# Kernel optimization log

Hardware: AMD Instinct MI355X
Metric: run time of the kernel (lower is better)

The kernel has to match this reference:

```python
import jax, jax.numpy as jnp
import numpy as np

N = 50000        # nodes
E = 800000       # edges (avg degree 16)
F_IN = 128       # in_channels
HID = 32         # hidden_channels per head
H = 8            # heads
DH = HID * H     # 256, concat dim
NC = {'TL': 12, 'YL': 30, 'TS': 60, 'TZ': 120}
NEG_SLOPE = 0.2  # PyG GATConv default


def setup_inputs() -> dict:
    key = jax.random.key(0)
    ks = jax.random.split(key, 40)
    rn = lambda k, s, sc=0.1: jax.random.normal(k, s, jnp.float32) * sc
    inp = {}
    inp['x'] = jax.random.normal(ks[0], (N, F_IN), jnp.float32)
    inp['edge_index'] = jax.random.randint(ks[1], (2, E), 0, N, dtype=jnp.int64)
    # conv1: in -> H x HID (concat)
    inp['W1'] = rn(ks[2], (F_IN, DH)); inp['a1s'] = rn(ks[3], (H, HID)); inp['a1d'] = rn(ks[4], (H, HID)); inp['b1'] = jnp.zeros((DH,), jnp.float32)
    # conv2: DH -> H x HID (concat)
    inp['W2'] = rn(ks[5], (DH, DH)); inp['a2s'] = rn(ks[6], (H, HID)); inp['a2d'] = rn(ks[7], (H, HID)); inp['b2'] = jnp.zeros((DH,), jnp.float32)
    # task heads: DH -> C, heads=1, concat=False
    i = 8
    for t, c in NC.items():
        inp['W_' + t] = rn(ks[i], (DH, c)); i += 1
        inp['as_' + t] = rn(ks[i], (1, c)); i += 1
        inp['ad_' + t] = rn(ks[i], (1, c)); i += 1
        inp['b_' + t] = jnp.zeros((c,), jnp.float32)
    return inp


def gat_conv(x, src, dst, W, a_s, a_d, b, concat):
    """PyG-style GATConv (eval mode, self-loops already in src/dst)."""
    n = x.shape[0]
    heads, out_ch = a_s.shape
    h = (x @ W).reshape(n, heads, out_ch)                 # [N,H,C]
    alpha_s = jnp.einsum('nhc,hc->nh', h, a_s)            # [N,H]
    alpha_d = jnp.einsum('nhc,hc->nh', h, a_d)
    e = jax.nn.leaky_relu(alpha_s[src] + alpha_d[dst], NEG_SLOPE)   # [E,H]
    # numerically-stable segment softmax over incoming edges of each dst
    m = jax.ops.segment_max(e, dst, num_segments=n)
    ex = jnp.exp(e - m[dst])
    denom = jax.ops.segment_sum(ex, dst, num_segments=n)
    alpha = ex / (denom[dst] + 1e-16)                     # [E,H]
    out = jax.ops.segment_sum(alpha[:, :, None] * h[src], dst, num_segments=n)  # [N,H,C]
    out = out.reshape(n, heads * out_ch) if concat else out.mean(axis=1)
    return out + b


def reference(x, edge_index, W1, a1s, a1d, b1, W2, a2s, a2d, b2,
              W_TL, as_TL, ad_TL, b_TL, W_YL, as_YL, ad_YL, b_YL,
              W_TS, as_TS, ad_TS, b_TS, W_TZ, as_TZ, ad_TZ, b_TZ):
    n = x.shape[0]
    loop = jnp.arange(n, dtype=edge_index.dtype)
    src = jnp.concatenate([edge_index[0], loop])
    dst = jnp.concatenate([edge_index[1], loop])
    h = jax.nn.elu(gat_conv(x, src, dst, W1, a1s, a1d, b1, True))
    h = gat_conv(h, src, dst, W2, a2s, a2d, b2, True)
    tl = jax.nn.log_softmax(gat_conv(h, src, dst, W_TL, as_TL, ad_TL, b_TL, False), axis=1)
    yl = jax.nn.log_softmax(gat_conv(h, src, dst, W_YL, as_YL, ad_YL, b_YL, False), axis=1)
    ts = jax.nn.log_softmax(gat_conv(h, src, dst, W_TS, as_TS, ad_TS, b_TS, False), axis=1)
    tz = jax.nn.log_softmax(gat_conv(h, src, dst, W_TZ, as_TZ, ad_TZ, b_TZ, False), axis=1)
    return (tl, yl, ts, tz)
```

## Files before the change

kernel.cpp:

```cpp
#include <hip/hip_runtime.h>
#include <math.h>


#define NEG_SLOPE 0.2f

typedef short s8v __attribute__((ext_vector_type(8)));
typedef short s4v __attribute__((ext_vector_type(4)));
typedef float f4v __attribute__((ext_vector_type(4)));

__device__ __forceinline__ short f2bf(float x) {
    unsigned u = __float_as_uint(x);
    u += 0x7fffu + ((u >> 16) & 1u);
    return (short)(u >> 16);
}
__device__ __forceinline__ float bf2f(short b) {
    return __uint_as_float(((unsigned)(unsigned short)b) << 16);
}
__device__ __forceinline__ void split2(float x, short& h, short& l) {
    h = f2bf(x);
    l = f2bf(x - bf2f(h));
}
__device__ __forceinline__ float4 bf4_to_f4(s4v v) {
    return make_float4(bf2f(v[0]), bf2f(v[1]), bf2f(v[2]), bf2f(v[3]));
}


__global__ void init_kernel(int* __restrict__ deg, int* __restrict__ cursor, int n) {
    int i = blockIdx.x * blockDim.x + threadIdx.x;
    if (i < n) { deg[i] = 1; cursor[i] = 0; }
}

__global__ void count_kernel(const int* __restrict__ dst, int* __restrict__ deg, int E) {
    int i = blockIdx.x * blockDim.x + threadIdx.x;
    if (i < E) atomicAdd(&deg[dst[i]], 1);
}

__global__ __launch_bounds__(1024) void scan_kernel(const int* __restrict__ deg,
                                                    int* __restrict__ rowstart, int n) {
    __shared__ int sh[1024];
    __shared__ int carry_sh;
    if (threadIdx.x == 0) { carry_sh = 0; rowstart[0] = 0; }
    __syncthreads();
    for (int base = 0; base < n; base += 8192) {
        int vals[8];
        int sum = 0;
        int i0 = base + threadIdx.x * 8;
        #pragma unroll
        for (int j = 0; j < 8; ++j) {
            int i = i0 + j;
            int v = (i < n) ? deg[i] : 0;
            sum += v;
            vals[j] = sum;
        }
        sh[threadIdx.x] = sum;
        __syncthreads();
        for (int off = 1; off < 1024; off <<= 1) {
            int t = (threadIdx.x >= (unsigned)off) ? sh[threadIdx.x - off] : 0;
            __syncthreads();
            sh[threadIdx.x] += t;
            __syncthreads();
        }
        int excl = sh[threadIdx.x] - sum + carry_sh;
        #pragma unroll
        for (int j = 0; j < 8; ++j) {
            int i = i0 + j;
            if (i < n) rowstart[i + 1] = excl + vals[j];
        }
        __syncthreads();
        if (threadIdx.x == 0) carry_sh += sh[1023];
        __syncthreads();
    }
}

__global__ void scatter_kernel(const int* __restrict__ src, const int* __restrict__ dst,
                               const int* __restrict__ rowstart, int* __restrict__ cursor,
                               int* __restrict__ csr, int* __restrict__ csrd, int E, int n) {
    int i = blockIdx.x * blockDim.x + threadIdx.x;
    if (i >= E + n) return;
    int s, d;
    if (i < E) { s = src[i]; d = dst[i]; }
    else       { s = d = i - E; }
    int p = atomicAdd(&cursor[d], 1);
    int slot = rowstart[d] + p;
    csr[slot] = s;
    csrd[slot] = d;
}


__global__ void tobf_kernel(const float* __restrict__ A, short* __restrict__ Ah, int n4) {
    int i = blockIdx.x * blockDim.x + threadIdx.x;
    if (i >= n4) return;
    float4 v = ((const float4*)A)[i];
    s4v hv = {f2bf(v.x), f2bf(v.y), f2bf(v.z), f2bf(v.w)};
    ((s4v*)Ah)[i] = hv;
}

__global__ void split_bt_kernel(const float* __restrict__ B, short* __restrict__ Bh,
                                short* __restrict__ Bl, int K, int Nc, int kshift) {
    int idx = blockIdx.x * blockDim.x + threadIdx.x;
    if (idx >= Nc * K) return;
    int n = idx >> kshift;
    int k = idx & (K - 1);
    float v = B[(size_t)k * Nc + n];
    short h, l; split2(v, h, l);
    Bh[idx] = h;
    Bl[idx] = l;
}

__global__ void fold_alpha8_kernel(const float* __restrict__ W,
                                   const float* __restrict__ a_s, const float* __restrict__ a_d,
                                   short* __restrict__ Bth, short* __restrict__ Btl,
                                   int K, int Nfeat) {
    int idx = blockIdx.x * blockDim.x + threadIdx.x;
    if (idx >= K * 16) return;
    int j = idx / K, k = idx % K;
    int h = j & 7;
    const float* av = ((j < 8) ? a_s : a_d) + h * 32;
    const float* wp = W + (size_t)k * 256 + h * 32;
    float s = 0.f;
    #pragma unroll
    for (int c = 0; c < 32; ++c) s += wp[c] * av[c];
    short hi, lo; split2(s, hi, lo);
    size_t off = (size_t)(Nfeat + j) * K + k;
    Bth[off] = hi; Btl[off] = lo;
}

__global__ void fold_alpha4_kernel(const float* __restrict__ Wcat,
                                   const float* __restrict__ ascat, const float* __restrict__ adcat,
                                   short* __restrict__ Bth, short* __restrict__ Btl) {
    int idx = blockIdx.x * blockDim.x + threadIdx.x;
    if (idx >= 256 * 8) return;
    int j = idx >> 8, k = idx & 255;
    const int CO[4] = {0, 12, 42, 102};
    const int CL[4] = {12, 30, 60, 120};
    int t = j & 3;
    const float* av = ((j < 4) ? ascat : adcat) + CO[t];
    const float* wp = Wcat + (size_t)k * 222 + CO[t];
    float s = 0.f;
    for (int c = 0; c < CL[t]; ++c) s += wp[c] * av[c];
    short hi, lo; split2(s, hi, lo);
    size_t off = (size_t)(222 + j) * 256 + k;
    Bth[off] = hi; Btl[off] = lo;
}


#define MB 128
#define NB 64
#define KS 32

__global__ __launch_bounds__(256) void gemm_mfma_kernel(
        const short* __restrict__ Ah_g,
        const short* __restrict__ Bth_g, const short* __restrict__ Btl_g,
        short* __restrict__ Cb, int cb_stride,
        float* __restrict__ als, float* __restrict__ ald, int nsplit,
        int M, int K, int Nfeat, int NcExt) {
    __shared__ __align__(16) short Ah[MB][40];
    __shared__ __align__(16) short Bh[NB][40];
    __shared__ __align__(16) short Bl[NB][40];

    int t = threadIdx.x;
    int lane = t & 63, w = t >> 6;
    int quad = lane >> 4, l16 = lane & 15;
    int row0 = blockIdx.y * MB, col0 = blockIdx.x * NB;

    f4v acc[2][4];
    #pragma unroll
    for (int mt = 0; mt < 2; ++mt)
        #pragma unroll
        for (int nt = 0; nt < 4; ++nt)
            acc[mt][nt] = (f4v){0.f, 0.f, 0.f, 0.f};

    for (int k0 = 0; k0 < K; k0 += KS) {
        __syncthreads();
        #pragma unroll
        for (int i = 0; i < 2; ++i) {
            int u = i * 256 + t;
            int r = u >> 2, kk = (u & 3) * 8;
            int gr = row0 + r;
            s8v vh = {0, 0, 0, 0, 0, 0, 0, 0};
            if (gr < M) vh = *(const s8v*)(Ah_g + (size_t)gr * K + k0 + kk);
            *(s8v*)&Ah[r][kk] = vh;
        }
        {
            int n = t >> 2, kk = (t & 3) * 8;
            int gc = col0 + n;
            s8v vh = {0, 0, 0, 0, 0, 0, 0, 0};
            s8v vl = {0, 0, 0, 0, 0, 0, 0, 0};
            if (gc < NcExt) {
                vh = *(const s8v*)(Bth_g + (size_t)gc * K + k0 + kk);
                vl = *(const s8v*)(Btl_g + (size_t)gc * K + k0 + kk);
            }
            *(s8v*)&Bh[n][kk] = vh;
            *(s8v*)&Bl[n][kk] = vl;
        }
        __syncthreads();

        int kb = quad * 8;
        s8v a_f[2], b_h[4], b_l[4];
        #pragma unroll
        for (int mt = 0; mt < 2; ++mt) {
            int r = w * 32 + mt * 16 + l16;
            a_f[mt] = *(const s8v*)&Ah[r][kb];
        }
        #pragma unroll
        for (int nt = 0; nt < 4; ++nt) {
            int c = nt * 16 + l16;
            b_h[nt] = *(const s8v*)&Bh[c][kb];
            b_l[nt] = *(const s8v*)&Bl[c][kb];
        }
        #pragma unroll
        for (int mt = 0; mt < 2; ++mt)
            #pragma unroll
            for (int nt = 0; nt < 4; ++nt) {
                acc[mt][nt] = __builtin_amdgcn_mfma_f32_16x16x32_bf16(
                    a_f[mt], b_h[nt], acc[mt][nt], 0, 0, 0);
                acc[mt][nt] = __builtin_amdgcn_mfma_f32_16x16x32_bf16(
                    a_f[mt], b_l[nt], acc[mt][nt], 0, 0, 0);
            }
    }

    #pragma unroll
    for (int mt = 0; mt < 2; ++mt) {
        #pragma unroll
        for (int nt = 0; nt < 4; ++nt) {
            int gc = col0 + nt * 16 + l16;
            if (gc >= NcExt) continue;
            #pragma unroll
            for (int r = 0; r < 4; ++r) {
                int gr = row0 + w * 32 + mt * 16 + quad * 4 + r;
                if (gr >= M) continue;
                float v = acc[mt][nt][r];
                if (gc < Nfeat) {
                    Cb[(size_t)gr * cb_stride + gc] = f2bf(v);
                } else {
                    int j = gc - Nfeat;
                    if (j < nsplit)            als[(size_t)gr * nsplit + j] = v;
                    else if (j < 2 * nsplit)   ald[(size_t)gr * nsplit + (j - nsplit)] = v;
                }
            }
        }
    }
}


__global__ void ew8_kernel(const float* __restrict__ als, const float* __restrict__ ald,
                           const int* __restrict__ csr, const int* __restrict__ csrd,
                           float* __restrict__ ew, int M) {
    int i = blockIdx.x * blockDim.x + threadIdx.x;
    if (i >= M) return;
    int s = csr[i], d = csrd[i];
    const float4* ap = (const float4*)(als + (size_t)s * 8);
    const float4* dp = (const float4*)(ald + (size_t)d * 8);
    float4 a0 = ap[0], a1 = ap[1];
    float4 d0 = dp[0], d1 = dp[1];
    float v[8] = {a0.x + d0.x, a0.y + d0.y, a0.z + d0.z, a0.w + d0.w,
                  a1.x + d1.x, a1.y + d1.y, a1.z + d1.z, a1.w + d1.w};
    float w[8];
    #pragma unroll
    for (int h = 0; h < 8; ++h) {
        float x = v[h];
        x = (x > 0.f) ? x : NEG_SLOPE * x;
        w[h] = __expf(x);
    }
    float4* op = (float4*)(ew + (size_t)i * 8);
    op[0] = make_float4(w[0], w[1], w[2], w[3]);
    op[1] = make_float4(w[4], w[5], w[6], w[7]);
}


__global__ __launch_bounds__(256) void gat_gather_kernel(
        const short* __restrict__ hb, const float* __restrict__ ew,
        const int* __restrict__ rowstart, const int* __restrict__ csr,
        const float* __restrict__ bias, short* __restrict__ oh, int n, int elu) {
    int wid  = blockIdx.x * 4 + (threadIdx.x >> 6);
    int lane = threadIdx.x & 63;
    if (wid >= n) return;
    int row = rowstart[wid];
    int deg = rowstart[wid + 1] - row;
    int hp = lane >> 3;
    int ch = lane * 4;
    const int* cp = csr + row;
    const float* wp = ew + (size_t)row * 8 + hp;

    float4 acc = {0.f, 0.f, 0.f, 0.f};
    float wsum = 0.f;
    int e = 0;
    for (; e + 4 <= deg; e += 4) {
        int s0 = cp[e], s1 = cp[e + 1], s2 = cp[e + 2], s3 = cp[e + 3];
        float w0 = wp[(size_t)(e + 0) * 8];
        float w1 = wp[(size_t)(e + 1) * 8];
        float w2 = wp[(size_t)(e + 2) * 8];
        float w3 = wp[(size_t)(e + 3) * 8];
        float4 h0 = bf4_to_f4(*(const s4v*)(hb + (size_t)s0 * 256 + ch));
        float4 h1 = bf4_to_f4(*(const s4v*)(hb + (size_t)s1 * 256 + ch));
        float4 h2 = bf4_to_f4(*(const s4v*)(hb + (size_t)s2 * 256 + ch));
        float4 h3 = bf4_to_f4(*(const s4v*)(hb + (size_t)s3 * 256 + ch));
        acc.x += w0 * h0.x + w1 * h1.x + w2 * h2.x + w3 * h3.x;
        acc.y += w0 * h0.y + w1 * h1.y + w2 * h2.y + w3 * h3.y;
        acc.z += w0 * h0.z + w1 * h1.z + w2 * h2.z + w3 * h3.z;
        acc.w += w0 * h0.w + w1 * h1.w + w2 * h2.w + w3 * h3.w;
        wsum += (w0 + w1) + (w2 + w3);
    }
    for (; e < deg; ++e) {
        int s0 = cp[e];
        float w0 = wp[(size_t)e * 8];
        float4 h0 = bf4_to_f4(*(const s4v*)(hb + (size_t)s0 * 256 + ch));
        acc.x += w0 * h0.x; acc.y += w0 * h0.y;
        acc.z += w0 * h0.z; acc.w += w0 * h0.w;
        wsum += w0;
    }
    float inv = 1.f / (wsum + 1e-16f);
    float4 b4 = *(const float4*)(bias + ch);
    float v[4] = {acc.x * inv + b4.x, acc.y * inv + b4.y,
                  acc.z * inv + b4.z, acc.w * inv + b4.w};
    if (elu) {
        #pragma unroll
        for (int j = 0; j < 4; ++j)
            v[j] = (v[j] > 0.f) ? v[j] : __expf(v[j]) - 1.f;
    }
    s4v hv = {f2bf(v[0]), f2bf(v[1]), f2bf(v[2]), f2bf(v[3])};
    *(s4v*)(oh + (size_t)wid * 256 + ch) = hv;
}


__global__ void pack_w_kernel(const float* __restrict__ wTL, const float* __restrict__ wYL,
                              const float* __restrict__ wTS, const float* __restrict__ wTZ,
                              const float* __restrict__ bTL, const float* __restrict__ bYL,
                              const float* __restrict__ bTS, const float* __restrict__ bTZ,
                              const float* __restrict__ asTL, const float* __restrict__ asYL,
                              const float* __restrict__ asTS, const float* __restrict__ asTZ,
                              const float* __restrict__ adTL, const float* __restrict__ adYL,
                              const float* __restrict__ adTS, const float* __restrict__ adTZ,
                              float* __restrict__ Wcat, float* __restrict__ bcat,
                              float* __restrict__ ascat, float* __restrict__ adcat) {
    int idx = blockIdx.x * blockDim.x + threadIdx.x;
    if (idx < 256 * 222) {
        int r = idx / 222, c = idx % 222;
        float v;
        if (c < 12)       v = wTL[r * 12 + c];
        else if (c < 42)  v = wYL[r * 30 + (c - 12)];
        else if (c < 102) v = wTS[r * 60 + (c - 42)];
        else              v = wTZ[r * 120 + (c - 102)];
        Wcat[idx] = v;
    }
    if (idx < 222) {
        bcat[idx]  = (idx < 12) ? bTL[idx] : (idx < 42) ? bYL[idx - 12]
                   : (idx < 102) ? bTS[idx - 42] : bTZ[idx - 102];
        ascat[idx] = (idx < 12) ? asTL[idx] : (idx < 42) ? asYL[idx - 12]
                   : (idx < 102) ? asTS[idx - 42] : asTZ[idx - 102];
        adcat[idx] = (idx < 12) ? adTL[idx] : (idx < 42) ? adYL[idx - 12]
                   : (idx < 102) ? adTS[idx - 42] : adTZ[idx - 102];
    }
}


__global__ void ew4_kernel(const float* __restrict__ ast, const float* __restrict__ adt,
                           const int* __restrict__ csr, const int* __restrict__ csrd,
                           float* __restrict__ ew, int M) {
    int i = blockIdx.x * blockDim.x + threadIdx.x;
    if (i >= M) return;
    int s = csr[i], d = csrd[i];
    float4 a = *(const float4*)(ast + (size_t)s * 4);
    float4 b = *(const float4*)(adt + (size_t)d * 4);
    float v[4] = {a.x + b.x, a.y + b.y, a.z + b.z, a.w + b.w};
    float w[4];
    #pragma unroll
    for (int t = 0; t < 4; ++t) {
        float x = v[t];
        x = (x > 0.f) ? x : NEG_SLOPE * x;
        w[t] = __expf(x);
    }
    *(float4*)(ew + (size_t)i * 4) = make_float4(w[0], w[1], w[2], w[3]);
}


__device__ __forceinline__ float sel4(int t, float v0, float v1, float v2, float v3) {
    return (t == 0) ? v0 : (t == 1) ? v1 : (t == 2) ? v2 : v3;
}
__device__ __forceinline__ int sel4i(int t, int v0, int v1, int v2, int v3) {
    return (t == 0) ? v0 : (t == 1) ? v1 : (t == 2) ? v2 : v3;
}

__global__ __launch_bounds__(256) void task_gather_ls_kernel(
        const short* __restrict__ htb, const float* __restrict__ ew,
        const int* __restrict__ rowstart, const int* __restrict__ csr,
        const float* __restrict__ bcat, float* __restrict__ out, int n) {
    int wid  = blockIdx.x * 4 + (threadIdx.x >> 6);
    int lane = threadIdx.x & 63;
    if (wid >= n) return;
    int row = rowstart[wid];
    int deg = rowstart[wid + 1] - row;
    int ch0 = lane * 4;

    bool valj[4]; bool lo_j[4];
    int t_lo, t_hi;
    {
        int tj0 = (ch0 >= 102) ? 3 : (ch0 >= 42) ? 2 : (ch0 >= 12) ? 1 : 0;
        int ch3 = ch0 + 3;
        int tj3 = (ch3 >= 102) ? 3 : (ch3 >= 42) ? 2 : (ch3 >= 12) ? 1 : 0;
        t_lo = tj0; t_hi = tj3;
        #pragma unroll
        for (int j = 0; j < 4; ++j) {
            int ch = ch0 + j;
            valj[j] = (ch < 222);
            int tj = (ch >= 102) ? 3 : (ch >= 42) ? 2 : (ch >= 12) ? 1 : 0;
            lo_j[j] = (tj == t_lo);
        }
    }

    const int* cp = csr + row;
    const float* wp = ew + (size_t)row * 4;

    float acc[4] = {0.f, 0.f, 0.f, 0.f};
    float ws_lo = 0.f, ws_hi = 0.f;
    int e = 0;
    for (; e + 4 <= deg; e += 4) {
        int s0 = cp[e], s1 = cp[e + 1], s2 = cp[e + 2], s3 = cp[e + 3];
        float wlo0 = wp[(size_t)(e + 0) * 4 + t_lo], whi0 = wp[(size_t)(e + 0) * 4 + t_hi];
        float wlo1 = wp[(size_t)(e + 1) * 4 + t_lo], whi1 = wp[(size_t)(e + 1) * 4 + t_hi];
        float wlo2 = wp[(size_t)(e + 2) * 4 + t_lo], whi2 = wp[(size_t)(e + 2) * 4 + t_hi];
        float wlo3 = wp[(size_t)(e + 3) * 4 + t_lo], whi3 = wp[(size_t)(e + 3) * 4 + t_hi];
        float4 h0 = bf4_to_f4(*(const s4v*)(htb + (size_t)s0 * 224 + ch0));
        float4 h1 = bf4_to_f4(*(const s4v*)(htb + (size_t)s1 * 224 + ch0));
        float4 h2 = bf4_to_f4(*(const s4v*)(htb + (size_t)s2 * 224 + ch0));
        float4 h3 = bf4_to_f4(*(const s4v*)(htb + (size_t)s3 * 224 + ch0));
        ws_lo += (wlo0 + wlo1) + (wlo2 + wlo3);
        ws_hi += (whi0 + whi1) + (whi2 + whi3);
        float hv0[4] = {h0.x, h0.y, h0.z, h0.w};
        float hv1[4] = {h1.x, h1.y, h1.z, h1.w};
        float hv2[4] = {h2.x, h2.y, h2.z, h2.w};
        float hv3[4] = {h3.x, h3.y, h3.z, h3.w};
        #pragma unroll
        for (int j = 0; j < 4; ++j) {
            float w0 = lo_j[j] ? wlo0 : whi0;
            float w1 = lo_j[j] ? wlo1 : whi1;
            float w2 = lo_j[j] ? wlo2 : whi2;
            float w3 = lo_j[j] ? wlo3 : whi3;
            acc[j] += w0 * hv0[j] + w1 * hv1[j] + w2 * hv2[j] + w3 * hv3[j];
        }
    }
    for (; e < deg; ++e) {
        int s = cp[e];
        float wlo = wp[(size_t)e * 4 + t_lo];
        float whi = wp[(size_t)e * 4 + t_hi];
        ws_lo += wlo; ws_hi += whi;
        float4 h0 = bf4_to_f4(*(const s4v*)(htb + (size_t)s * 224 + ch0));
        float hv[4] = {h0.x, h0.y, h0.z, h0.w};
        #pragma unroll
        for (int j = 0; j < 4; ++j)
            acc[j] += (lo_j[j] ? wlo : whi) * hv[j];
    }
    float inv_lo = 1.f / (ws_lo + 1e-16f);
    float inv_hi = 1.f / (ws_hi + 1e-16f);

    float vout[4];
    float m_lo = -1e30f, m_hi = -1e30f;
    #pragma unroll
    for (int j = 0; j < 4; ++j) {
        float v = 0.f;
        if (valj[j]) {
            v = acc[j] * (lo_j[j] ? inv_lo : inv_hi) + bcat[ch0 + j];
            if (lo_j[j]) m_lo = fmaxf(m_lo, v); else m_hi = fmaxf(m_hi, v);
        }
        vout[j] = v;
    }
    float m0 = -1e30f, m1 = -1e30f, m2 = -1e30f, m3 = -1e30f;
    m0 = (t_lo == 0) ? fmaxf(m0, m_lo) : m0;  m0 = (t_hi == 0) ? fmaxf(m0, m_hi) : m0;
    m1 = (t_lo == 1) ? fmaxf(m1, m_lo) : m1;  m1 = (t_hi == 1) ? fmaxf(m1, m_hi) : m1;
    m2 = (t_lo == 2) ? fmaxf(m2, m_lo) : m2;  m2 = (t_hi == 2) ? fmaxf(m2, m_hi) : m2;
    m3 = (t_lo == 3) ? fmaxf(m3, m_lo) : m3;  m3 = (t_hi == 3) ? fmaxf(m3, m_hi) : m3;
    #pragma unroll
    for (int off = 1; off < 64; off <<= 1) {
        m0 = fmaxf(m0, __shfl_xor(m0, off));
        m1 = fmaxf(m1, __shfl_xor(m1, off));
        m2 = fmaxf(m2, __shfl_xor(m2, off));
        m3 = fmaxf(m3, __shfl_xor(m3, off));
    }
    float mt_lo = sel4(t_lo, m0, m1, m2, m3);
    float mt_hi = sel4(t_hi, m0, m1, m2, m3);
    float s_lo = 0.f, s_hi = 0.f;
    #pragma unroll
    for (int j = 0; j < 4; ++j) {
        if (valj[j]) {
            if (lo_j[j]) s_lo += __expf(vout[j] - mt_lo);
            else         s_hi += __expf(vout[j] - mt_hi);
        }
    }
    float s0 = ((t_lo == 0) ? s_lo : 0.f) + ((t_hi == 0 && t_hi != t_lo) ? s_hi : 0.f);
    float s1 = ((t_lo == 1) ? s_lo : 0.f) + ((t_hi == 1 && t_hi != t_lo) ? s_hi : 0.f);
    float s2 = ((t_lo == 2) ? s_lo : 0.f) + ((t_hi == 2 && t_hi != t_lo) ? s_hi : 0.f);
    float s3 = ((t_lo == 3) ? s_lo : 0.f) + ((t_hi == 3 && t_hi != t_lo) ? s_hi : 0.f);
    #pragma unroll
    for (int off = 1; off < 64; off <<= 1) {
        s0 += __shfl_xor(s0, off);
        s1 += __shfl_xor(s1, off);
        s2 += __shfl_xor(s2, off);
        s3 += __shfl_xor(s3, off);
    }
    float l0 = m0 + __logf(s0), l1 = m1 + __logf(s1);
    float l2 = m2 + __logf(s2), l3 = m3 + __logf(s3);
    float lse_lo = sel4(t_lo, l0, l1, l2, l3);
    float lse_hi = sel4(t_hi, l0, l1, l2, l3);
    int co_lo = sel4i(t_lo, 0, 12, 42, 102), cl_lo = sel4i(t_lo, 12, 30, 60, 120);
    int co_hi = sel4i(t_hi, 0, 12, 42, 102), cl_hi = sel4i(t_hi, 12, 30, 60, 120);
    #pragma unroll
    for (int j = 0; j < 4; ++j) {
        if (!valj[j]) continue;
        int co = lo_j[j] ? co_lo : co_hi;
        int cl = lo_j[j] ? cl_lo : cl_hi;
        float lse = lo_j[j] ? lse_lo : lse_hi;
        out[(size_t)co * n + (size_t)wid * cl + (ch0 + j - co)] = vout[j] - lse;
    }
}


extern "C" void kernel_launch(void* const* d_in, const int* in_sizes, int n_in,
                              void* d_out, int out_size, void* d_ws, size_t ws_size,
                              hipStream_t stream) {
    const float* x   = (const float*)d_in[0];
    const int*   ei  = (const int*)d_in[1];
    const float* W1  = (const float*)d_in[2];
    const float* a1s = (const float*)d_in[3];
    const float* a1d = (const float*)d_in[4];
    const float* b1  = (const float*)d_in[5];
    const float* W2  = (const float*)d_in[6];
    const float* a2s = (const float*)d_in[7];
    const float* a2d = (const float*)d_in[8];
    const float* b2  = (const float*)d_in[9];
    const float* W_TL = (const float*)d_in[10]; const float* as_TL = (const float*)d_in[11];
    const float* ad_TL = (const float*)d_in[12]; const float* b_TL = (const float*)d_in[13];
    const float* W_YL = (const float*)d_in[14]; const float* as_YL = (const float*)d_in[15];
    const float* ad_YL = (const float*)d_in[16]; const float* b_YL = (const float*)d_in[17];
    const float* W_TS = (const float*)d_in[18]; const float* as_TS = (const float*)d_in[19];
    const float* ad_TS = (const float*)d_in[20]; const float* b_TS = (const float*)d_in[21];
    const float* W_TZ = (const float*)d_in[22]; const float* as_TZ = (const float*)d_in[23];
    const float* ad_TZ = (const float*)d_in[24]; const float* b_TZ = (const float*)d_in[25];

    const int N = in_sizes[0] / 128;
    const int E = in_sizes[1] / 2;
    const int* e_src = ei;
    const int* e_dst = ei + E;
    const int M = E + N;

    float* ws = (float*)d_ws;
    float* B1   = ws;
    float* B2   = B1 + (size_t)N * 256;
    float* B3   = B2 + (size_t)N * 256;
    float* as1  = B3 + (size_t)N * 256;
    float* ad1  = as1 + (size_t)N * 8;
    float* as2  = ad1 + (size_t)N * 8;
    float* ad2  = as2 + (size_t)N * 8;
    float* ast  = ad2 + (size_t)N * 8;
    float* adt  = ast + (size_t)N * 4;
    float* Wcat = adt + (size_t)N * 4;
    float* bcat = Wcat + 256 * 222;
    float* ascat = bcat + 224;
    float* adcat = ascat + 224;
    int* deg      = (int*)(adcat + 224);
    int* rowstart = deg + N;
    int* cursor   = rowstart + (N + 1);
    int* csr      = cursor + N;
    int* csrd     = csr + M;
    uintptr_t wsp = (uintptr_t)(csrd + M);
    wsp = (wsp + 15) & ~(uintptr_t)15;
    short* W1h = (short*)wsp;
    short* W1l = W1h + 272 * 128;
    short* W2h = W1l + 272 * 128;
    short* W2l = W2h + 272 * 256;
    short* Wth = W2l + 272 * 256;
    short* Wtl = Wth + 230 * 256;
    short* Xh  = (short*)B1;
    short* Sh  = (short*)B1;
    short* Th  = (short*)B1;
    short* h1b = (short*)B2;
    short* h2b = (short*)B2;
    short* htb = (short*)B2;
    float* ew1 = B3;
    float* ew2 = B3;
    float* ewt = B3;

    float* out = (float*)d_out;

    const int B = 256;
    init_kernel<<<(N + B - 1) / B, B, 0, stream>>>(deg, cursor, N);
    count_kernel<<<(E + B - 1) / B, B, 0, stream>>>(e_dst, deg, E);
    scan_kernel<<<1, 1024, 0, stream>>>(deg, rowstart, N);
    scatter_kernel<<<(M + B - 1) / B, B, 0, stream>>>(e_src, e_dst, rowstart, cursor, csr, csrd, E, N);
    pack_w_kernel<<<(256 * 222 + B - 1) / B, B, 0, stream>>>(W_TL, W_YL, W_TS, W_TZ,
        b_TL, b_YL, b_TS, b_TZ, as_TL, as_YL, as_TS, as_TZ, ad_TL, ad_YL, ad_TS, ad_TZ,
        Wcat, bcat, ascat, adcat);
    split_bt_kernel<<<(256 * 128 + B - 1) / B, B, 0, stream>>>(W1, W1h, W1l, 128, 256, 7);
    split_bt_kernel<<<(256 * 256 + B - 1) / B, B, 0, stream>>>(W2, W2h, W2l, 256, 256, 8);
    split_bt_kernel<<<(222 * 256 + B - 1) / B, B, 0, stream>>>(Wcat, Wth, Wtl, 256, 222, 8);
    fold_alpha8_kernel<<<(128 * 16 + B - 1) / B, B, 0, stream>>>(W1, a1s, a1d, W1h, W1l, 128, 256);
    fold_alpha8_kernel<<<(256 * 16 + B - 1) / B, B, 0, stream>>>(W2, a2s, a2d, W2h, W2l, 256, 256);
    fold_alpha4_kernel<<<(256 * 8 + B - 1) / B, B, 0, stream>>>(Wcat, ascat, adcat, Wth, Wtl);
    tobf_kernel<<<((N * 128 / 4) + B - 1) / B, B, 0, stream>>>(x, Xh, N * 128 / 4);
    {
        dim3 g((272 + NB - 1) / NB, (N + MB - 1) / MB);
        gemm_mfma_kernel<<<g, 256, 0, stream>>>(Xh, W1h, W1l, h1b, 256,
                                                as1, ad1, 8, N, 128, 256, 272);
    }
    ew8_kernel<<<(M + B - 1) / B, B, 0, stream>>>(as1, ad1, csr, csrd, ew1, M);
    gat_gather_kernel<<<(N + 3) / 4, 256, 0, stream>>>(h1b, ew1, rowstart, csr, b1, Sh, N, 1);
    {
        dim3 g((272 + NB - 1) / NB, (N + MB - 1) / MB);
        gemm_mfma_kernel<<<g, 256, 0, stream>>>(Sh, W2h, W2l, h2b, 256,
                                                as2, ad2, 8, N, 256, 256, 272);
    }
    ew8_kernel<<<(M + B - 1) / B, B, 0, stream>>>(as2, ad2, csr, csrd, ew2, M);
    gat_gather_kernel<<<(N + 3) / 4, 256, 0, stream>>>(h2b, ew2, rowstart, csr, b2, Th, N, 0);
    {
        dim3 g((230 + NB - 1) / NB, (N + MB - 1) / MB);
        gemm_mfma_kernel<<<g, 256, 0, stream>>>(Th, Wth, Wtl, htb, 224,
                                                ast, adt, 4, N, 256, 222, 230);
    }
    ew4_kernel<<<(M + B - 1) / B, B, 0, stream>>>(ast, adt, csr, csrd, ewt, M);
    task_gather_ls_kernel<<<(N + 3) / 4, 256, 0, stream>>>(htb, ewt, rowstart, csr, bcat, out, N);
}
```

Before: 642.7 us.

## Pad CSR rows to multiples of four and vectorize gather index loads

Each CSR row is padded to a multiple of four entries. Padding slots hold -1 sources, which get zero edge weights and clamp to node 0 in the gathers. This lets the gather loops load indices as int4, drop the scalar remainder loop, and make the source indices wave-uniform through readfirstlane. The block scan is also rewritten to use wave shuffles instead of a shared-memory Hillis-Steele scan. The cost is a memset of the enlarged CSR arrays, more edge-weight slots to compute, and wasted gather work on padded entries.

```diff
diff --git a/kernel.cpp b/kernel.cpp
--- a/kernel.cpp
+++ b/kernel.cpp
@@ -23,6 +23,10 @@
 __device__ __forceinline__ float4 bf4_to_f4(s4v v) {
     return make_float4(bf2f(v[0]), bf2f(v[1]), bf2f(v[2]), bf2f(v[3]));
 }
+__device__ __forceinline__ int rfl_clamp(int v) {
+    int s = __builtin_amdgcn_readfirstlane(v);
+    return s < 0 ? 0 : s;
+}
 
 
 __global__ void init_kernel(int* __restrict__ deg, int* __restrict__ cursor, int n) {
@@ -37,8 +41,9 @@
 
 __global__ __launch_bounds__(1024) void scan_kernel(const int* __restrict__ deg,
                                                     int* __restrict__ rowstart, int n) {
-    __shared__ int sh[1024];
+    __shared__ int wsum[16];
     __shared__ int carry_sh;
+    int lane = threadIdx.x & 63, wv = threadIdx.x >> 6;
     if (threadIdx.x == 0) { carry_sh = 0; rowstart[0] = 0; }
     __syncthreads();
     for (int base = 0; base < n; base += 8192) {
@@ -48,26 +53,37 @@
         #pragma unroll
         for (int j = 0; j < 8; ++j) {
             int i = i0 + j;
-            int v = (i < n) ? deg[i] : 0;
+            int v = (i < n) ? ((deg[i] + 3) & ~3) : 0;
             sum += v;
             vals[j] = sum;
         }
-        sh[threadIdx.x] = sum;
+        int incl = sum;
+        #pragma unroll
+        for (int off = 1; off < 64; off <<= 1) {
+            int t = __shfl_up(incl, off);
+            if (lane >= off) incl += t;
+        }
+        if (lane == 63) wsum[wv] = incl;
         __syncthreads();
-        for (int off = 1; off < 1024; off <<= 1) {
-            int t = (threadIdx.x >= (unsigned)off) ? sh[threadIdx.x - off] : 0;
-            __syncthreads();
-            sh[threadIdx.x] += t;
-            __syncthreads();
-        }
-        int excl = sh[threadIdx.x] - sum + carry_sh;
+        if (wv == 0) {
+            int s = (lane < 16) ? wsum[lane] : 0;
+            #pragma unroll
+            for (int off = 1; off < 16; off <<= 1) {
+                int t = __shfl_up(s, off);
+                if (lane >= off) s += t;
+            }
+            if (lane < 16) wsum[lane] = s;
+        }
+        __syncthreads();
+        int wexcl = (wv == 0) ? 0 : wsum[wv - 1];
+        int excl = carry_sh + wexcl + (incl - sum);
         #pragma unroll
         for (int j = 0; j < 8; ++j) {
             int i = i0 + j;
             if (i < n) rowstart[i + 1] = excl + vals[j];
         }
         __syncthreads();
-        if (threadIdx.x == 0) carry_sh += sh[1023];
+        if (threadIdx.x == 0) carry_sh += wsum[15];
         __syncthreads();
     }
 }
@@ -245,10 +261,16 @@
 
 __global__ void ew8_kernel(const float* __restrict__ als, const float* __restrict__ ald,
                            const int* __restrict__ csr, const int* __restrict__ csrd,
-                           float* __restrict__ ew, int M) {
+                           float* __restrict__ ew, int M4) {
     int i = blockIdx.x * blockDim.x + threadIdx.x;
-    if (i >= M) return;
+    if (i >= M4) return;
     int s = csr[i], d = csrd[i];
+    float4* op = (float4*)(ew + (size_t)i * 8);
+    if (s < 0) {
+        op[0] = make_float4(0.f, 0.f, 0.f, 0.f);
+        op[1] = make_float4(0.f, 0.f, 0.f, 0.f);
+        return;
+    }
     const float4* ap = (const float4*)(als + (size_t)s * 8);
     const float4* dp = (const float4*)(ald + (size_t)d * 8);
     float4 a0 = ap[0], a1 = ap[1];
@@ -262,7 +284,6 @@
         x = (x > 0.f) ? x : NEG_SLOPE * x;
         w[h] = __expf(x);
     }
-    float4* op = (float4*)(ew + (size_t)i * 8);
     op[0] = make_float4(w[0], w[1], w[2], w[3]);
     op[1] = make_float4(w[4], w[5], w[6], w[7]);
 }
@@ -276,7 +297,7 @@
     int lane = threadIdx.x & 63;
     if (wid >= n) return;
     int row = rowstart[wid];
-    int deg = rowstart[wid + 1] - row;
+    int pdeg = rowstart[wid + 1] - row;
     int hp = lane >> 3;
     int ch = lane * 4;
     const int* cp = csr + row;
@@ -284,9 +305,12 @@
 
     float4 acc = {0.f, 0.f, 0.f, 0.f};
     float wsum = 0.f;
-    int e = 0;
-    for (; e + 4 <= deg; e += 4) {
-        int s0 = cp[e], s1 = cp[e + 1], s2 = cp[e + 2], s3 = cp[e + 3];
+    for (int e = 0; e < pdeg; e += 4) {
+        int4 sv = *(const int4*)(cp + e);
+        int s0 = rfl_clamp(sv.x);
+        int s1 = rfl_clamp(sv.y);
+        int s2 = rfl_clamp(sv.z);
+        int s3 = rfl_clamp(sv.w);
         float w0 = wp[(size_t)(e + 0) * 8];
         float w1 = wp[(size_t)(e + 1) * 8];
         float w2 = wp[(size_t)(e + 2) * 8];
@@ -300,14 +324,6 @@
         acc.z += w0 * h0.z + w1 * h1.z + w2 * h2.z + w3 * h3.z;
         acc.w += w0 * h0.w + w1 * h1.w + w2 * h2.w + w3 * h3.w;
         wsum += (w0 + w1) + (w2 + w3);
-    }
-    for (; e < deg; ++e) {
-        int s0 = cp[e];
-        float w0 = wp[(size_t)e * 8];
-        float4 h0 = bf4_to_f4(*(const s4v*)(hb + (size_t)s0 * 256 + ch));
-        acc.x += w0 * h0.x; acc.y += w0 * h0.y;
-        acc.z += w0 * h0.z; acc.w += w0 * h0.w;
-        wsum += w0;
     }
     float inv = 1.f / (wsum + 1e-16f);
     float4 b4 = *(const float4*)(bias + ch);
@@ -356,10 +372,14 @@
 
 __global__ void ew4_kernel(const float* __restrict__ ast, const float* __restrict__ adt,
                            const int* __restrict__ csr, const int* __restrict__ csrd,
-                           float* __restrict__ ew, int M) {
+                           float* __restrict__ ew, int M4) {
     int i = blockIdx.x * blockDim.x + threadIdx.x;
-    if (i >= M) return;
+    if (i >= M4) return;
     int s = csr[i], d = csrd[i];
+    if (s < 0) {
+        *(float4*)(ew + (size_t)i * 4) = make_float4(0.f, 0.f, 0.f, 0.f);
+        return;
+    }
     float4 a = *(const float4*)(ast + (size_t)s * 4);
     float4 b = *(const float4*)(adt + (size_t)d * 4);
     float v[4] = {a.x + b.x, a.y + b.y, a.z + b.z, a.w + b.w};
@@ -389,7 +409,7 @@
     int lane = threadIdx.x & 63;
     if (wid >= n) return;
     int row = rowstart[wid];
-    int deg = rowstart[wid + 1] - row;
+    int pdeg = rowstart[wid + 1] - row;
     int ch0 = lane * 4;
 
     bool valj[4]; bool lo_j[4];
@@ -413,9 +433,12 @@
 
     float acc[4] = {0.f, 0.f, 0.f, 0.f};
     float ws_lo = 0.f, ws_hi = 0.f;
-    int e = 0;
-    for (; e + 4 <= deg; e += 4) {
-        int s0 = cp[e], s1 = cp[e + 1], s2 = cp[e + 2], s3 = cp[e + 3];
+    for (int e = 0; e < pdeg; e += 4) {
+        int4 sv = *(const int4*)(cp + e);
+        int s0 = rfl_clamp(sv.x);
+        int s1 = rfl_clamp(sv.y);
+        int s2 = rfl_clamp(sv.z);
+        int s3 = rfl_clamp(sv.w);
         float wlo0 = wp[(size_t)(e + 0) * 4 + t_lo], whi0 = wp[(size_t)(e + 0) * 4 + t_hi];
         float wlo1 = wp[(size_t)(e + 1) * 4 + t_lo], whi1 = wp[(size_t)(e + 1) * 4 + t_hi];
         float wlo2 = wp[(size_t)(e + 2) * 4 + t_lo], whi2 = wp[(size_t)(e + 2) * 4 + t_hi];
@@ -438,17 +461,6 @@
             float w3 = lo_j[j] ? wlo3 : whi3;
             acc[j] += w0 * hv0[j] + w1 * hv1[j] + w2 * hv2[j] + w3 * hv3[j];
         }
-    }
-    for (; e < deg; ++e) {
-        int s = cp[e];
-        float wlo = wp[(size_t)e * 4 + t_lo];
-        float whi = wp[(size_t)e * 4 + t_hi];
-        ws_lo += wlo; ws_hi += whi;
-        float4 h0 = bf4_to_f4(*(const s4v*)(htb + (size_t)s * 224 + ch0));
-        float hv[4] = {h0.x, h0.y, h0.z, h0.w};
-        #pragma unroll
-        for (int j = 0; j < 4; ++j)
-            acc[j] += (lo_j[j] ? wlo : whi) * hv[j];
     }
     float inv_lo = 1.f / (ws_lo + 1e-16f);
     float inv_hi = 1.f / (ws_hi + 1e-16f);
@@ -540,7 +552,7 @@
     const int E = in_sizes[1] / 2;
     const int* e_src = ei;
     const int* e_dst = ei + E;
-    const int M = E + N;
+    const int M4 = E + 4 * N;
 
     float* ws = (float*)d_ws;
     float* B1   = ws;
@@ -558,10 +570,10 @@
     float* adcat = ascat + 224;
     int* deg      = (int*)(adcat + 224);
     int* rowstart = deg + N;
-    int* cursor   = rowstart + (N + 1);
+    int* cursor   = rowstart + (N + 4);
     int* csr      = cursor + N;
-    int* csrd     = csr + M;
-    uintptr_t wsp = (uintptr_t)(csrd + M);
+    int* csrd     = csr + M4;
+    uintptr_t wsp = (uintptr_t)(csrd + M4);
     wsp = (wsp + 15) & ~(uintptr_t)15;
     short* W1h = (short*)wsp;
     short* W1l = W1h + 272 * 128;
@@ -585,7 +597,8 @@
     init_kernel<<<(N + B - 1) / B, B, 0, stream>>>(deg, cursor, N);
     count_kernel<<<(E + B - 1) / B, B, 0, stream>>>(e_dst, deg, E);
     scan_kernel<<<1, 1024, 0, stream>>>(deg, rowstart, N);
-    scatter_kernel<<<(M + B - 1) / B, B, 0, stream>>>(e_src, e_dst, rowstart, cursor, csr, csrd, E, N);
+    hipMemsetAsync(csr, 0xFF, (size_t)2 * M4 * sizeof(int), stream);
+    scatter_kernel<<<(E + N + B - 1) / B, B, 0, stream>>>(e_src, e_dst, rowstart, cursor, csr, csrd, E, N);
     pack_w_kernel<<<(256 * 222 + B - 1) / B, B, 0, stream>>>(W_TL, W_YL, W_TS, W_TZ,
         b_TL, b_YL, b_TS, b_TZ, as_TL, as_YL, as_TS, as_TZ, ad_TL, ad_YL, ad_TS, ad_TZ,
         Wcat, bcat, ascat, adcat);
@@ -601,20 +614,20 @@
         gemm_mfma_kernel<<<g, 256, 0, stream>>>(Xh, W1h, W1l, h1b, 256,
                                                 as1, ad1, 8, N, 128, 256, 272);
     }
-    ew8_kernel<<<(M + B - 1) / B, B, 0, stream>>>(as1, ad1, csr, csrd, ew1, M);
+    ew8_kernel<<<(M4 + B - 1) / B, B, 0, stream>>>(as1, ad1, csr, csrd, ew1, M4);
     gat_gather_kernel<<<(N + 3) / 4, 256, 0, stream>>>(h1b, ew1, rowstart, csr, b1, Sh, N, 1);
     {
         dim3 g((272 + NB - 1) / NB, (N + MB - 1) / MB);
         gemm_mfma_kernel<<<g, 256, 0, stream>>>(Sh, W2h, W2l, h2b, 256,
                                                 as2, ad2, 8, N, 256, 256, 272);
     }
-    ew8_kernel<<<(M + B - 1) / B, B, 0, stream>>>(as2, ad2, csr, csrd, ew2, M);
+    ew8_kernel<<<(M4 + B - 1) / B, B, 0, stream>>>(as2, ad2, csr, csrd, ew2, M4);
     gat_gather_kernel<<<(N + 3) / 4, 256, 0, stream>>>(h2b, ew2, rowstart, csr, b2, Th, N, 0);
     {
         dim3 g((230 + NB - 1) / NB, (N + MB - 1) / MB);
         gemm_mfma_kernel<<<g, 256, 0, stream>>>(Th, Wth, Wtl, htb, 224,
                                                 ast, adt, 4, N, 256, 222, 230);
     }
-    ew4_kernel<<<(M + B - 1) / B, B, 0, stream>>>(ast, adt, csr, csrd, ewt, M);
+    ew4_kernel<<<(M4 + B - 1) / B, B, 0, stream>>>(ast, adt, csr, csrd, ewt, M4);
     task_gather_ls_kernel<<<(N + 3) / 4, 256, 0, stream>>>(htb, ewt, rowstart, csr, bcat, out, N);
 }
```

Result: faster. 629.6 us (-2.0%).
